# Kernel optimization log

Hardware: AMD Instinct MI355X
Metric: run time of the kernel (lower is better)

The kernel has to match this reference:

```python
import jax, jax.numpy as jnp
import numpy as np

C = 512
K = 3
DIL = 1
EPS = 1e-6


def weight_quant(w):
    # BitNet b1.58 ternary quantization with straight-through estimator:
    # scale = mean(|w|); w_q = clamp(round(w/scale), -1, 1) * scale
    s = jnp.maximum(jnp.mean(jnp.abs(w)), 1e-5)
    q = jnp.clip(jnp.round(w / s), -1.0, 1.0) * s
    return w + jax.lax.stop_gradient(q - w)


def conv1d(x, w, b, padding, dilation):
    # x: [B, C, L], w: [O, I, K]
    y = jax.lax.conv_general_dilated(
        x, w, window_strides=(1,), padding=[(padding, padding)],
        rhs_dilation=(dilation,), dimension_numbers=("NCH", "OIH", "NCH"))
    return y + b[None, :, None]


def setup_inputs() -> dict:
    key = jax.random.key(0)
    k0, k1, k2, k3, k4 = jax.random.split(key, 5)
    fan_in = C * K
    lim = 1.0 / np.sqrt(fan_in)
    x = jax.random.normal(k0, (16, C, 4096), dtype=jnp.float32)
    w1 = jax.random.uniform(k1, (C, C, K), jnp.float32, -lim, lim)
    b1 = jax.random.uniform(k2, (C,), jnp.float32, -lim, lim)
    w2 = jax.random.uniform(k3, (C, C, K), jnp.float32, -lim, lim)
    b2 = jax.random.uniform(k4, (C,), jnp.float32, -lim, lim)
    g = jnp.ones((C,), dtype=jnp.float32)  # RMSNorm gain
    return {"x": x, "w1": w1, "b1": b1, "w2": w2, "b2": b2, "g": g}


def reference(x, w1, b1, w2, b2, g):
    residual = x
    # RMSNorm over channel axis (original transposes to [B,L,C], norms last dim)
    ms = jnp.mean(jnp.square(x), axis=1, keepdims=True)
    h = x * jax.lax.rsqrt(ms + EPS) * g[None, :, None]
    h = jax.nn.silu(h)
    p1 = (K * DIL - DIL) // 2
    h = conv1d(h, weight_quant(w1), b1, p1, DIL)
    h = jax.nn.silu(h)
    h = conv1d(h, weight_quant(w2), b2, K // 2, 1)
    return h + residual
```

## Files before the change

kernel.cpp:

```cpp
#include <hip/hip_runtime.h>

#define BATCH 16
#define CCH 512
#define LEN 4096
#define LPAD 4098

typedef unsigned short u16;
typedef __bf16 bf16x8 __attribute__((ext_vector_type(8)));
typedef float f32x4 __attribute__((ext_vector_type(4)));
typedef u16 u16x8 __attribute__((ext_vector_type(8)));
typedef u16 u16x4 __attribute__((ext_vector_type(4)));

__device__ __forceinline__ u16 f2bf(float f) {
    unsigned u = __float_as_uint(f);
    u = (u + 0x7fffu + ((u >> 16) & 1u)) >> 16;
    return (u16)u;
}
__device__ __forceinline__ float bf2f(u16 v) {
    return __uint_as_float(((unsigned)v) << 16);
}
__device__ __forceinline__ float silu_f(float v) {
    return v / (1.f + __expf(-v));
}
__device__ __forceinline__ void async16(const u16* g, u16* l) {
    __builtin_amdgcn_global_load_lds(
        (const __attribute__((address_space(1))) unsigned int*)g,
        (__attribute__((address_space(3))) unsigned int*)l, 16, 0, 0);
}

#define SBAR() __builtin_amdgcn_sched_barrier(0)
#define HWBAR() { SBAR(); __builtin_amdgcn_s_barrier(); SBAR(); }
#define WAIT_LGKM0() { asm volatile("s_waitcnt lgkmcnt(0)" ::: "memory"); SBAR(); }
#define WAIT_VM(n) { asm volatile("s_waitcnt vmcnt(" #n ")" ::: "memory"); SBAR(); }

__global__ __launch_bounds__(256)
void absmean_partial(const float* __restrict__ w1, const float* __restrict__ w2,
                     float* __restrict__ part) {
    const int tid = threadIdx.x;
    const int base = blockIdx.x * 3072;
    float s1 = 0.f, s2 = 0.f;
    for (int i = tid; i < 3072; i += 256) {
        s1 += fabsf(w1[base + i]);
        s2 += fabsf(w2[base + i]);
    }
    __shared__ float r1[256], r2[256];
    r1[tid] = s1; r2[tid] = s2;
    __syncthreads();
    for (int off = 128; off > 0; off >>= 1) {
        if (tid < off) { r1[tid] += r1[tid + off]; r2[tid] += r2[tid + off]; }
        __syncthreads();
    }
    if (tid == 0) { part[blockIdx.x] = r1[0]; part[256 + blockIdx.x] = r2[0]; }
}

__global__ __launch_bounds__(256)
void finalize_scale(const float* __restrict__ part, float* __restrict__ sv) {
    const int tid = threadIdx.x;
    __shared__ float r1[256], r2[256];
    r1[tid] = part[tid]; r2[tid] = part[256 + tid];
    __syncthreads();
    for (int off = 128; off > 0; off >>= 1) {
        if (tid < off) { r1[tid] += r1[tid + off]; r2[tid] += r2[tid + off]; }
        __syncthreads();
    }
    if (tid == 0) {
        sv[0] = fmaxf(r1[0] * (1.f / 786432.f), 1e-5f);
        sv[1] = fmaxf(r2[0] * (1.f / 786432.f), 1e-5f);
    }
}

__global__ __launch_bounds__(256)
void quantize_w(const float* __restrict__ w, const float* __restrict__ sv,
                int sidx, u16* __restrict__ wqt) {
    const int idx = blockIdx.x * 256 + threadIdx.x;
    const float s = sv[sidx];
    float q = rintf(w[idx] / s);
    q = fmaxf(-1.f, fminf(1.f, q));
    const int o   = idx / 1536;
    const int rem = idx - o * 1536;
    const int i   = rem / 3;
    const int k   = rem - i * 3;
    wqt[k * (CCH * CCH) + o * CCH + i] = f2bf(q);
}

__global__ __launch_bounds__(256)
void zero_pads(u16* __restrict__ h, u16* __restrict__ h1) {
    const int idx = blockIdx.x * 256 + threadIdx.x;
    const int b = idx >> 10;
    const int r = (idx >> 9) & 1;
    const int i = idx & 511;
    const size_t off = ((size_t)b * LPAD + (r ? (LPAD - 1) : 0)) * CCH + i;
    h[off] = 0;
    h1[off] = 0;
}

__global__ __launch_bounds__(256)
void rms_silu_transpose(const float* __restrict__ x, const float* __restrict__ g,
                        u16* __restrict__ h_t) {
    __shared__ u16   xt[CCH][33];
    __shared__ float red[8][32];
    __shared__ float rinv[32];
    const int tid = threadIdx.x;
    const int bb  = blockIdx.x >> 7;
    const int l0  = (blockIdx.x & 127) << 5;

    const size_t xbase = (size_t)bb * CCH * LEN + l0;
    {
        const int i_hi = tid >> 3;
        const int l4   = (tid & 7) << 2;
        #pragma unroll
        for (int it = 0; it < 16; ++it) {
            const int i = it * 32 + i_hi;
            const float4 v = *(const float4*)&x[xbase + (size_t)i * LEN + l4];
            xt[i][l4 + 0] = f2bf(v.x);
            xt[i][l4 + 1] = f2bf(v.y);
            xt[i][l4 + 2] = f2bf(v.z);
            xt[i][l4 + 3] = f2bf(v.w);
        }
    }
    __syncthreads();
    {
        const int l = tid & 31, seg = tid >> 5;
        const int ibeg = seg * 64;
        float ss = 0.f;
        #pragma unroll 8
        for (int i = ibeg; i < ibeg + 64; ++i) {
            const float v = bf2f(xt[i][l]);
            ss += v * v;
        }
        red[seg][l] = ss;
    }
    __syncthreads();
    if (tid < 32) {
        float tot = 0.f;
        #pragma unroll
        for (int k2 = 0; k2 < 8; ++k2) tot += red[k2][tid];
        rinv[tid] = rsqrtf(tot * (1.f / 512.f) + 1e-6f);
    }
    __syncthreads();
    {
        const int l  = tid >> 3;
        const int i0 = (tid & 7) << 6;
        const float ri = rinv[l];
        const size_t ob = ((size_t)bb * LPAD + l0 + l + 1) * CCH + i0;
        for (int ii = 0; ii < 64; ii += 8) {
            u16x8 ov;
            #pragma unroll
            for (int jj = 0; jj < 8; ++jj) {
                const int i = i0 + ii + jj;
                float v = bf2f(xt[i][l]) * ri * g[i];
                ov[jj] = f2bf(silu_f(v));
            }
            *(u16x8*)&h_t[ob + ii] = ov;
        }
    }
}

template<int EPI>
__global__ __launch_bounds__(512)
void conv_gemm8(const u16* __restrict__ Bsrc, const u16* __restrict__ Wq,
                const float* __restrict__ sptr, const float* __restrict__ bias,
                const float* __restrict__ resid, u16* __restrict__ outb,
                float* __restrict__ outf) {
    extern __shared__ u16 lds[];
    const int tid  = threadIdx.x;
    const int lane = tid & 63;
    const int wave = tid >> 6;
    const int wm = wave >> 1;
    const int wn = wave & 1;

    const int wgid = (blockIdx.x & 7) * 128 + (blockIdx.x >> 3);
    const int mt = wgid & 1;
    const int nt = wgid >> 1;
    const int o0 = mt << 8;
    const int bb = nt >> 5;
    const int l0 = (nt & 31) << 7;

    const int sr   = tid >> 2;
    const int scol = ((tid & 3) << 3) ^ ((sr & 3) << 3);
    const int sdst = tid << 3;

    const u16* aSrcBase = Wq + (size_t)(o0 + sr) * CCH + scol;
    const u16* bSrcBase = Bsrc + ((size_t)bb * LPAD + l0 + sr) * CCH + scol;

    auto stage_full = [&](int pb, int t) {
        const int ks = t % 3;
        const int i0 = (t / 3) << 5;
        const u16* wsrc = aSrcBase + ks * (CCH * CCH) + i0;
        async16(wsrc, &lds[pb * 12288 + sdst]);
        async16(wsrc + 128 * CCH, &lds[pb * 12288 + 4096 + sdst]);
        async16(bSrcBase + (size_t)ks * CCH + i0, &lds[pb * 12288 + 8192 + sdst]);
    };

    const int cc = (((lane >> 4) ^ (lane & 3)) << 3);
    const int aOff = (wm * 64 + (lane & 15)) * 32 + cc;
    const int bOff = 8192 + (wn * 64 + (lane & 15)) * 32 + cc;

    f32x4 acc[4][4];
    #pragma unroll
    for (int m = 0; m < 4; ++m)
        #pragma unroll
        for (int n = 0; n < 4; ++n)
            acc[m][n] = (f32x4){0.f, 0.f, 0.f, 0.f};

    stage_full(0, 0);
    stage_full(1, 1);
    WAIT_VM(3);
    HWBAR();

    int pb = 0;
    for (int t = 0; t < 48; ++t) {
        const int cb = pb * 12288;
        const bool full = (t < 46);
        if (full) stage_full((pb + 2) % 3, t + 2);
        bf16x8 ar[4], br[4];
        #pragma unroll
        for (int m = 0; m < 4; ++m)
            ar[m] = *(const bf16x8*)&lds[cb + aOff + m * 512];
        #pragma unroll
        for (int n = 0; n < 4; ++n)
            br[n] = *(const bf16x8*)&lds[cb + bOff + n * 512];
        __builtin_amdgcn_s_setprio(1);
        #pragma unroll
        for (int m = 0; m < 4; ++m)
            #pragma unroll
            for (int n = 0; n < 4; ++n)
                acc[m][n] = __builtin_amdgcn_mfma_f32_16x16x32_bf16(
                    ar[m], br[n], acc[m][n], 0, 0, 0);
        __builtin_amdgcn_s_setprio(0);
        WAIT_LGKM0();
        if (full) { WAIT_VM(3); } else { WAIT_VM(0); }
        HWBAR();
        pb = (pb + 1) % 3;
    }

    const float sc = sptr[0];

    if (EPI == 1) {
        #pragma unroll
        for (int m = 0; m < 4; ++m) {
            const int o_loc = wm * 64 + m * 16 + ((lane >> 4) << 2);
            const int ob = o0 + o_loc;
            const float b0 = bias[ob + 0], b1 = bias[ob + 1];
            const float b2 = bias[ob + 2], b3 = bias[ob + 3];
            #pragma unroll
            for (int n = 0; n < 4; ++n) {
                const int l_loc = wn * 64 + n * 16 + (lane & 15);
                const f32x4 a = acc[m][n];
                u16x4 ov;
                ov[0] = f2bf(silu_f(sc * a[0] + b0));
                ov[1] = f2bf(silu_f(sc * a[1] + b1));
                ov[2] = f2bf(silu_f(sc * a[2] + b2));
                ov[3] = f2bf(silu_f(sc * a[3] + b3));
                char* p = (char*)lds + l_loc * 512 +
                          (((unsigned)(o_loc << 1)) ^ ((l_loc & 7) << 4));
                *(u16x4*)p = ov;
            }
        }
        __syncthreads();
        const int l_r = tid >> 2;
        const int oq  = (tid & 3) << 3;
        u16* gdst = outb + ((size_t)bb * LPAD + l0 + l_r + 1) * CCH + o0 + oq;
        char* srp = (char*)lds + l_r * 512;
        const int swz2 = (l_r & 7) << 4;
        #pragma unroll
        for (int c = 0; c < 8; ++c) {
            const uint4 v = *(const uint4*)(srp + (((oq << 1) + c * 64) ^ swz2));
            *(uint4*)(gdst + c * 32) = v;
        }
    } else {
        const int lbase = l0 + wn * 64 + (lane & 15);
        const int obase = o0 + wm * 64 + ((lane >> 4) << 2);
        #pragma unroll
        for (int m = 0; m < 4; ++m) {
            const int ob = obase + m * 16;
            #pragma unroll
            for (int n = 0; n < 4; ++n) {
                const int l = lbase + n * 16;
                const f32x4 a = acc[m][n];
                #pragma unroll
                for (int jj = 0; jj < 4; ++jj) {
                    const size_t idx = ((size_t)bb * CCH + (ob + jj)) * LEN + l;
                    outf[idx] = sc * a[jj] + bias[ob + jj] + resid[idx];
                }
            }
        }
    }
}

extern "C" void kernel_launch(void* const* d_in, const int* in_sizes, int n_in,
                              void* d_out, int out_size, void* d_ws, size_t ws_size,
                              hipStream_t stream) {
    const float* x  = (const float*)d_in[0];
    const float* w1 = (const float*)d_in[1];
    const float* b1 = (const float*)d_in[2];
    const float* w2 = (const float*)d_in[3];
    const float* b2 = (const float*)d_in[4];
    const float* g  = (const float*)d_in[5];
    float* out = (float*)d_out;

    char* ws = (char*)d_ws;
    float* sv   = (float*)ws;
    float* part = (float*)(ws + 256);
    u16* wq1   = (u16*)(ws + 4096);
    u16* wq2   = (u16*)(ws + 4096 + 1572864);
    u16* h_t   = (u16*)(ws + 4096 + 2 * 1572864);
    u16* h1_t  = (u16*)(ws + 4096 + 2 * 1572864 + 67141632);

    hipFuncSetAttribute((const void*)conv_gemm8<1>,
                        hipFuncAttributeMaxDynamicSharedMemorySize, 73728);
    hipFuncSetAttribute((const void*)conv_gemm8<2>,
                        hipFuncAttributeMaxDynamicSharedMemorySize, 73728);

    absmean_partial<<<dim3(256), dim3(256), 0, stream>>>(w1, w2, part);
    finalize_scale<<<dim3(1), dim3(256), 0, stream>>>(part, sv);
    quantize_w<<<dim3(3072), dim3(256), 0, stream>>>(w1, sv, 0, wq1);
    quantize_w<<<dim3(3072), dim3(256), 0, stream>>>(w2, sv, 1, wq2);
    zero_pads<<<dim3(64), dim3(256), 0, stream>>>(h_t, h1_t);
    rms_silu_transpose<<<dim3(2048), dim3(256), 0, stream>>>(x, g, h_t);
    conv_gemm8<1><<<dim3(1024), dim3(512), 73728, stream>>>(h_t, wq1, sv, b1,
                                                            nullptr, h1_t, nullptr);
    conv_gemm8<2><<<dim3(1024), dim3(512), 73728, stream>>>(h1_t, wq2, sv + 1, b2,
                                                            x, nullptr, out);
}
```

Before: 328.8 us.

## Use 4-wave blocks with 128x64 per-wave tiles and two blocks per CU

```diff
diff --git a/kernel.cpp b/kernel.cpp
--- a/kernel.cpp
+++ b/kernel.cpp
@@ -157,7 +157,7 @@
 }
 
 template<int EPI>
-__global__ __launch_bounds__(512)
+__global__ __launch_bounds__(256, 2)
 void conv_gemm8(const u16* __restrict__ Bsrc, const u16* __restrict__ Wq,
                 const float* __restrict__ sptr, const float* __restrict__ bias,
                 const float* __restrict__ resid, u16* __restrict__ outb,
@@ -176,70 +176,77 @@
     const int bb = nt >> 5;
     const int l0 = (nt & 31) << 7;
 
-    const int sr   = tid >> 2;
-    const int scol = ((tid & 3) << 3) ^ ((sr & 3) << 3);
+    const u16* aSrcBase = Wq + (size_t)(o0 + (tid >> 2)) * CCH + ((tid & 3) << 3);
+    const u16* bSrcBase = Bsrc + ((size_t)bb * LPAD + l0 + (tid >> 2)) * CCH +
+                          ((tid & 3) << 3);
     const int sdst = tid << 3;
-
-    const u16* aSrcBase = Wq + (size_t)(o0 + sr) * CCH + scol;
-    const u16* bSrcBase = Bsrc + ((size_t)bb * LPAD + l0 + sr) * CCH + scol;
 
     auto stage_full = [&](int pb, int t) {
         const int ks = t % 3;
         const int i0 = (t / 3) << 5;
         const u16* wsrc = aSrcBase + ks * (CCH * CCH) + i0;
-        async16(wsrc, &lds[pb * 12288 + sdst]);
-        async16(wsrc + 128 * CCH, &lds[pb * 12288 + 4096 + sdst]);
-        async16(bSrcBase + (size_t)ks * CCH + i0, &lds[pb * 12288 + 8192 + sdst]);
+        u16* const ad = &lds[pb * 12288 + sdst];
+        #pragma unroll
+        for (int j = 0; j < 4; ++j)
+            async16(wsrc + j * 64 * CCH, ad + j * 2048);
+        const u16* bsrc = bSrcBase + (size_t)ks * CCH + i0;
+        u16* const bd = &lds[pb * 12288 + 8192 + sdst];
+        #pragma unroll
+        for (int j = 0; j < 2; ++j)
+            async16(bsrc + (size_t)j * 64 * CCH, bd + j * 2048);
     };
 
-    const int cc = (((lane >> 4) ^ (lane & 3)) << 3);
-    const int aOff = (wm * 64 + (lane & 15)) * 32 + cc;
-    const int bOff = 8192 + (wn * 64 + (lane & 15)) * 32 + cc;
-
-    f32x4 acc[4][4];
+    const int co   = (lane >> 4) << 3;
+    const int aOff = wm * 4096 + (lane & 15) * 32 + co;
+    const int bOff = 8192 + wn * 2048 + (lane & 15) * 32 + co;
+
+    f32x4 acc[8][4];
     #pragma unroll
-    for (int m = 0; m < 4; ++m)
+    for (int m = 0; m < 8; ++m)
         #pragma unroll
         for (int n = 0; n < 4; ++n)
             acc[m][n] = (f32x4){0.f, 0.f, 0.f, 0.f};
 
     stage_full(0, 0);
     stage_full(1, 1);
-    WAIT_VM(3);
+    WAIT_VM(6);
     HWBAR();
 
     int pb = 0;
     for (int t = 0; t < 48; ++t) {
+        const bool full = (t < 46);
+        if (full) {
+            int nb = pb + 2; if (nb >= 3) nb -= 3;
+            stage_full(nb, t + 2);
+        }
         const int cb = pb * 12288;
-        const bool full = (t < 46);
-        if (full) stage_full((pb + 2) % 3, t + 2);
-        bf16x8 ar[4], br[4];
-        #pragma unroll
-        for (int m = 0; m < 4; ++m)
+        bf16x8 ar[8], br[4];
+        #pragma unroll
+        for (int m = 0; m < 8; ++m)
             ar[m] = *(const bf16x8*)&lds[cb + aOff + m * 512];
         #pragma unroll
         for (int n = 0; n < 4; ++n)
             br[n] = *(const bf16x8*)&lds[cb + bOff + n * 512];
         __builtin_amdgcn_s_setprio(1);
         #pragma unroll
-        for (int m = 0; m < 4; ++m)
+        for (int m = 0; m < 8; ++m)
             #pragma unroll
             for (int n = 0; n < 4; ++n)
                 acc[m][n] = __builtin_amdgcn_mfma_f32_16x16x32_bf16(
                     ar[m], br[n], acc[m][n], 0, 0, 0);
         __builtin_amdgcn_s_setprio(0);
         WAIT_LGKM0();
-        if (full) { WAIT_VM(3); } else { WAIT_VM(0); }
+        if (full) { WAIT_VM(6); } else { WAIT_VM(0); }
         HWBAR();
-        pb = (pb + 1) % 3;
+        ++pb; if (pb == 3) pb = 0;
     }
 
     const float sc = sptr[0];
 
     if (EPI == 1) {
         #pragma unroll
-        for (int m = 0; m < 4; ++m) {
-            const int o_loc = wm * 64 + m * 16 + ((lane >> 4) << 2);
+        for (int m = 0; m < 8; ++m) {
+            const int o_loc = wm * 128 + m * 16 + ((lane >> 4) << 2);
             const int ob = o0 + o_loc;
             const float b0 = bias[ob + 0], b1 = bias[ob + 1];
             const float b2 = bias[ob + 2], b3 = bias[ob + 3];
@@ -258,21 +265,24 @@
             }
         }
         __syncthreads();
-        const int l_r = tid >> 2;
-        const int oq  = (tid & 3) << 3;
-        u16* gdst = outb + ((size_t)bb * LPAD + l0 + l_r + 1) * CCH + o0 + oq;
-        char* srp = (char*)lds + l_r * 512;
-        const int swz2 = (l_r & 7) << 4;
-        #pragma unroll
-        for (int c = 0; c < 8; ++c) {
-            const uint4 v = *(const uint4*)(srp + (((oq << 1) + c * 64) ^ swz2));
-            *(uint4*)(gdst + c * 32) = v;
+        const int oq = (tid & 3) << 3;
+        #pragma unroll
+        for (int pass = 0; pass < 2; ++pass) {
+            const int lr = (tid >> 2) + pass * 64;
+            u16* gdst = outb + ((size_t)bb * LPAD + l0 + lr + 1) * CCH + o0 + oq;
+            char* srp = (char*)lds + lr * 512;
+            const int swz2 = (lr & 7) << 4;
+            #pragma unroll
+            for (int c = 0; c < 8; ++c) {
+                const uint4 v = *(const uint4*)(srp + ((oq * 2 + c * 64) ^ swz2));
+                *(uint4*)(gdst + c * 32) = v;
+            }
         }
     } else {
         const int lbase = l0 + wn * 64 + (lane & 15);
-        const int obase = o0 + wm * 64 + ((lane >> 4) << 2);
-        #pragma unroll
-        for (int m = 0; m < 4; ++m) {
+        const int obase = o0 + wm * 128 + ((lane >> 4) << 2);
+        #pragma unroll
+        for (int m = 0; m < 8; ++m) {
             const int ob = obase + m * 16;
             #pragma unroll
             for (int n = 0; n < 4; ++n) {
@@ -318,8 +328,8 @@
     quantize_w<<<dim3(3072), dim3(256), 0, stream>>>(w2, sv, 1, wq2);
     zero_pads<<<dim3(64), dim3(256), 0, stream>>>(h_t, h1_t);
     rms_silu_transpose<<<dim3(2048), dim3(256), 0, stream>>>(x, g, h_t);
-    conv_gemm8<1><<<dim3(1024), dim3(512), 73728, stream>>>(h_t, wq1, sv, b1,
+    conv_gemm8<1><<<dim3(1024), dim3(256), 73728, stream>>>(h_t, wq1, sv, b1,
                                                             nullptr, h1_t, nullptr);
-    conv_gemm8<2><<<dim3(1024), dim3(512), 73728, stream>>>(h1_t, wq2, sv + 1, b2,
+    conv_gemm8<2><<<dim3(1024), dim3(256), 73728, stream>>>(h1_t, wq2, sv + 1, b2,
                                                             x, nullptr, out);
 }
```

After: 331.6 us. Within noise of the previous version (+0.8%).
